# Optimization experiments

Measured on AMD Instinct MI355X. Metric: run time of the kernel, lower is better.

## Reference

```python
import jax, jax.numpy as jnp
import numpy as np
import math

D, S, B = 64, 2048, 16  # head_dim, seq_len, batch (inputs stored as [D, S, B])


def setup_inputs() -> dict:
    key = jax.random.key(0)
    kq, kk, kv = jax.random.split(key, 3)
    return {
        "Q": jax.random.normal(kq, (D, S, B), dtype=jnp.float32),
        "K": jax.random.normal(kk, (D, S, B), dtype=jnp.float32),
        "V": jax.random.normal(kv, (D, S, B), dtype=jnp.float32),
        "d_k": S,
    }


def reference(Q, K, V, d_k):
    # transpose(0, 2): [D, S, B] -> [B, S, D]
    q = jnp.transpose(Q, (2, 1, 0))
    k = jnp.transpose(K, (2, 1, 0))
    v = jnp.transpose(V, (2, 1, 0))
    # bmm(_Q, K_T) * 1/sqrt(d_k): [B, S, S]
    scores = jnp.einsum("bsd,btd->bst", q, k) * (1.0 / math.sqrt(d_k))
    # original does view(-1, d_k) + Softmax over dim=1; with d_k == last dim
    # this is a softmax over the key axis. Dropout is identity in eval mode.
    probs = jax.nn.softmax(scores, axis=-1)
    out = jnp.einsum("bst,btd->bsd", probs, v)  # [B, S, D]
    # transpose(0, 2) back: [D, S, B]
    return jnp.transpose(out, (2, 1, 0))
```

## Files before the change

kernel.cpp:

```cpp
#include <hip/hip_runtime.h>

#define D_ 64
#define S_ 2048
#define B_ 16
#define QT 64
#define KVT 128

typedef short short8 __attribute__((ext_vector_type(8)));
typedef short short4a __attribute__((ext_vector_type(4)));
typedef float floatx4 __attribute__((ext_vector_type(4)));
typedef unsigned uint2v __attribute__((ext_vector_type(2)));
typedef unsigned uint4v __attribute__((ext_vector_type(4)));

#define SC2 (1.4426950408889634f / 45.254833995939045f)

__device__ __forceinline__ unsigned short f2bf(float f) {
  unsigned u = __builtin_bit_cast(unsigned, f);
  u += 0x7fffu + ((u >> 16) & 1u);
  return (unsigned short)(u >> 16);
}

__global__ __launch_bounds__(256) void pack_all(const float* __restrict__ Q,
                                                const float* __restrict__ K,
                                                const float* __restrict__ V,
                                                unsigned short* __restrict__ Qp,
                                                unsigned short* __restrict__ Kp,
                                                unsigned short* __restrict__ Vt) {
  __shared__ __align__(16) unsigned short tile[256][72];
  const int t = threadIdx.x;
  const int bid = blockIdx.x;
  if (bid < 256) {
    const bool isK = bid >= 128;
    const float* src = isK ? K : Q;
    unsigned short* dst = isK ? Kp : Qp;
    const float scale = isK ? SC2 : 1.0f;
    const int rb = bid & 127;
    const int s0 = rb * 16;
#pragma unroll
    for (int i = 0; i < 16; i++) {
      int j = i * 256 + t;
      int d = j >> 6;
      int sb4 = (j & 63) * 4;
      const float4 v = *(const float4*)(src + (size_t)d * (S_ * B_) + s0 * B_ + sb4);
      float vv[4] = {v.x, v.y, v.z, v.w};
#pragma unroll
      for (int k = 0; k < 4; k++) {
        int sb = sb4 + k;
        tile[(sb & 15) * 16 + (sb >> 4)][d] = f2bf(vv[k] * scale);
      }
    }
    __syncthreads();
#pragma unroll
    for (int i = 0; i < 8; i++) {
      int j = i * 256 + t;
      int r = j >> 3, c = j & 7;
      int b = r >> 4, si = r & 15;
      uint4 v = *(const uint4*)(&tile[r][c * 8]);
      *(uint4*)(dst + (((size_t)(b * 128 + rb)) << 10) + ((c >> 2) << 9) +
                (((c & 3) * 16 + si) << 3)) = v;
    }
  } else {
    const int vb = bid - 256;
    const int s0 = (vb & 31) * 64;
    const int d0 = (vb >> 5) * 16;
    const int dblk = vb >> 5;
#pragma unroll
    for (int i = 0; i < 16; i++) {
      int j = i * 256 + t;
      int dd = j >> 8;
      int sb4 = (j & 255) * 4;
      const float4 v = *(const float4*)(V + (size_t)(d0 + dd) * (S_ * B_) + s0 * B_ + sb4);
      float vv[4] = {v.x, v.y, v.z, v.w};
#pragma unroll
      for (int k = 0; k < 4; k++) {
        int sb = sb4 + k;
        tile[(sb & 15) * 16 + dd][sb >> 4] = f2bf(vv[k]);
      }
    }
    __syncthreads();
#pragma unroll
    for (int i = 0; i < 8; i++) {
      int j = i * 256 + t;
      int b = j >> 7;
      int c32r = (j >> 6) & 1;
      int l = j & 63, g = l >> 4, ln = l & 15;
      const unsigned short* row = &tile[b * 16 + ln][c32r * 32];
      uint2 u0 = *(const uint2*)(row + g * 4);
      uint2 u1 = *(const uint2*)(row + 16 + g * 4);
      int c32 = (s0 >> 5) + c32r;
      uint4 o = make_uint4(u0.x, u0.y, u1.x, u1.y);
      *(uint4*)(Vt + (((size_t)(b * 64 + c32) * 4 + dblk) << 9) + l * 8) = o;
    }
  }
}

__global__ __launch_bounds__(256, 2) void attn(const unsigned short* __restrict__ Qp,
                                               const unsigned short* __restrict__ Kp,
                                               const unsigned short* __restrict__ Vt,
                                               float* __restrict__ Ot) {
  __shared__ __align__(16) char smem_[69632 + 1024];
  float* red = (float*)smem_;
  float* lred = (float*)(smem_ + 69632);

  const int tid = threadIdx.x;
  const int w = tid >> 6, l = tid & 63, g = l >> 4, ln = l & 15;
  const int b = blockIdx.x & 15;
  const int q0 = (int)(blockIdx.x >> 4) * QT;

  const unsigned short* Qb = Qp + ((size_t)b << 17);
  const unsigned short* Kb = Kp + ((size_t)b << 17);
  const unsigned short* Vb = Vt + ((size_t)b << 17);

  const unsigned short* Qw = Qb + (((size_t)(q0 >> 4)) << 10) + l * 8;
  const unsigned short* Kw = Kb + w * 2048 + l * 8;
  const unsigned short* Vw = Vb + w * 2048 + l * 8;

  short8 qf[4][2];
#pragma unroll
  for (int nf = 0; nf < 4; nf++)
#pragma unroll
    for (int ks = 0; ks < 2; ks++)
      qf[nf][ks] = *(const short8*)(Qw + nf * 1024 + ks * 512);

  short8 kf[2][2];
#pragma unroll
  for (int mf = 0; mf < 2; mf++)
#pragma unroll
    for (int ks = 0; ks < 2; ks++)
      kf[mf][ks] = *(const short8*)(Kw + mf * 1024 + ks * 512);

  short8 vf[4];
#pragma unroll
  for (int mfd = 0; mfd < 4; mfd++)
    vf[mfd] = *(const short8*)(Vw + mfd * 512);

  const short8 ones8 = {(short)0x3F80, (short)0x3F80, (short)0x3F80, (short)0x3F80,
                        (short)0x3F80, (short)0x3F80, (short)0x3F80, (short)0x3F80};
  floatx4 oacc[4][4];
  floatx4 dacc[4];
#pragma unroll
  for (int mfd = 0; mfd < 4; mfd++)
#pragma unroll
    for (int nf = 0; nf < 4; nf++) oacc[mfd][nf] = (floatx4){0.f, 0.f, 0.f, 0.f};
#pragma unroll
  for (int nf = 0; nf < 4; nf++) dacc[nf] = (floatx4){0.f, 0.f, 0.f, 0.f};

  for (int t = 0; t < 16; t++) {
    const int tn = ((t + 1) & 15) * 8192;

    floatx4 sacc[2][4];
#pragma unroll
    for (int mf = 0; mf < 2; mf++)
#pragma unroll
      for (int nf = 0; nf < 4; nf++) sacc[mf][nf] = (floatx4){0.f, 0.f, 0.f, 0.f};
    __builtin_amdgcn_s_setprio(1);
#pragma unroll
    for (int ks = 0; ks < 2; ks++)
#pragma unroll
      for (int mf = 0; mf < 2; mf++)
#pragma unroll
        for (int nf = 0; nf < 4; nf++)
          sacc[mf][nf] = __builtin_amdgcn_mfma_f32_16x16x32_bf16(kf[mf][ks], qf[nf][ks],
                                                                 sacc[mf][nf], 0, 0, 0);
    __builtin_amdgcn_s_setprio(0);

#pragma unroll
    for (int mf = 0; mf < 2; mf++)
#pragma unroll
      for (int ks = 0; ks < 2; ks++)
        kf[mf][ks] = *(const short8*)(Kw + tn + mf * 1024 + ks * 512);

    short8 pbf[4];
#pragma unroll
    for (int nf = 0; nf < 4; nf++) {
      uint2v pu[2];
#pragma unroll
      for (int mf = 0; mf < 2; mf++) {
        unsigned u0 = __builtin_bit_cast(unsigned, __builtin_amdgcn_exp2f(sacc[mf][nf][0])) + 0x8000u;
        unsigned u1 = __builtin_bit_cast(unsigned, __builtin_amdgcn_exp2f(sacc[mf][nf][1])) + 0x8000u;
        unsigned u2 = __builtin_bit_cast(unsigned, __builtin_amdgcn_exp2f(sacc[mf][nf][2])) + 0x8000u;
        unsigned u3 = __builtin_bit_cast(unsigned, __builtin_amdgcn_exp2f(sacc[mf][nf][3])) + 0x8000u;
        unsigned lo = __builtin_amdgcn_perm(u1, u0, 0x07060302u);
        unsigned hi = __builtin_amdgcn_perm(u3, u2, 0x07060302u);
        pu[mf] = (uint2v){lo, hi};
      }
      pbf[nf] = __builtin_bit_cast(short8, (uint4v){pu[0][0], pu[0][1], pu[1][0], pu[1][1]});
    }

    __builtin_amdgcn_s_setprio(1);
#pragma unroll
    for (int nf = 0; nf < 4; nf++)
      dacc[nf] = __builtin_amdgcn_mfma_f32_16x16x32_bf16(ones8, pbf[nf], dacc[nf], 0, 0, 0);

#pragma unroll
    for (int mfd = 0; mfd < 4; mfd++)
#pragma unroll
      for (int nf = 0; nf < 4; nf++)
        oacc[mfd][nf] = __builtin_amdgcn_mfma_f32_16x16x32_bf16(vf[mfd], pbf[nf],
                                                                oacc[mfd][nf], 0, 0, 0);
    __builtin_amdgcn_s_setprio(0);

#pragma unroll
    for (int mfd = 0; mfd < 4; mfd++)
      vf[mfd] = *(const short8*)(Vw + tn + mfd * 512);
  }

  if (g == 0) {
#pragma unroll
    for (int nf = 0; nf < 4; nf++) lred[w * 64 + nf * 16 + ln] = dacc[nf][0];
  }
#pragma unroll
  for (int mfd = 0; mfd < 4; mfd++)
#pragma unroll
    for (int nf = 0; nf < 4; nf++)
      *(floatx4*)(&red[w * 4352 + (nf * 16 + ln) * 68 + mfd * 16 + g * 4]) = oacc[mfd][nf];
  __syncthreads();

  const int q = l;
  const float denom = lred[q] + lred[64 + q] + lred[128 + q] + lred[192 + q];
  const float linv = 1.0f / denom;
#pragma unroll
  for (int i = 0; i < 4; i++) {
    floatx4 s = (floatx4){0.f, 0.f, 0.f, 0.f};
#pragma unroll
    for (int w2 = 0; w2 < 4; w2++)
      s += *(const floatx4*)(&red[w2 * 4352 + q * 68 + w * 16 + i * 4]);
    s *= linv;
#pragma unroll
    for (int r = 0; r < 4; r++)
      Ot[(size_t)(b * D_ + w * 16 + i * 4 + r) * S_ + q0 + q] = s[r];
  }
}

__global__ __launch_bounds__(256) void unpack_o(const float* __restrict__ Ot,
                                                float* __restrict__ out) {
  const int d0 = (int)(blockIdx.x & 7) * 8;
  const int s0 = (int)(blockIdx.x >> 3) * 64;
  __shared__ float u[8 * 1024];
  const int t = threadIdx.x;
#pragma unroll
  for (int i = 0; i < 8; i++) {
    int j = i * 256 + t;
    int d = j >> 8, bb = (j >> 4) & 15, c = j & 15;
    float4 v = *(const float4*)(Ot + (size_t)(bb * D_ + d0 + d) * S_ + s0 + c * 4);
    float vv[4] = {v.x, v.y, v.z, v.w};
#pragma unroll
    for (int k = 0; k < 4; k++) {
      int si = c * 4 + k;
      int W = si * 16 + bb;
      int Wp = W ^ ((si & 15) << 2);
      u[d * 1024 + Wp] = vv[k];
    }
  }
  __syncthreads();
#pragma unroll
  for (int i = 0; i < 8; i++) {
    int j = i * 256 + t;
    int d = j >> 8, c2 = j & 255;
    int G = c2 ^ ((c2 >> 2) & 15);
    float4 v = *(const float4*)(&u[d * 1024 + G * 4]);
    *(float4*)(out + (size_t)(d0 + d) * (S_ * B_) + s0 * B_ + c2 * 4) = v;
  }
}

extern "C" void kernel_launch(void* const* d_in, const int* in_sizes, int n_in,
                              void* d_out, int out_size, void* d_ws, size_t ws_size,
                              hipStream_t stream) {
  const float* Q = (const float*)d_in[0];
  const float* K = (const float*)d_in[1];
  const float* V = (const float*)d_in[2];
  float* out = (float*)d_out;
  char* ws = (char*)d_ws;
  unsigned short* Qp = (unsigned short*)(ws);
  unsigned short* Kp = (unsigned short*)(ws + (4u << 20));
  unsigned short* Vt = (unsigned short*)(ws + (8u << 20));
  float* Ot = (float*)(ws + (12u << 20));

  hipLaunchKernelGGL(pack_all, dim3(384), dim3(256), 0, stream, Q, K, V, Qp, Kp, Vt);
  hipLaunchKernelGGL(attn, dim3(512), dim3(256), 0, stream, Qp, Kp, Vt, Ot);
  hipLaunchKernelGGL(unpack_o, dim3(256), dim3(256), 0, stream, Ot, out);
}
```

Measured before the change: 100.0 us.

## Double query tile per block to 8 waves and halve LDS reduction buffer

Each attention block now handles 128 queries with 512 threads: two groups of four waves, each group splitting the key range four ways for its own 64-query half. The cross-wave output reduction is restructured into a two-stage add in shared memory, using half-sized buffers per query half, which cuts LDS use per query and removes the four-way reads in the final pass. The intent is to halve the block count and keep per-block LDS bounded so more waves stay resident. The cost is an extra barrier and read-modify-write traffic in the reduction.

```diff
diff --git a/kernel.cpp b/kernel.cpp
--- a/kernel.cpp
+++ b/kernel.cpp
@@ -3,11 +3,10 @@
 #define D_ 64
 #define S_ 2048
 #define B_ 16
-#define QT 64
+#define QT 128
 #define KVT 128
 
 typedef short short8 __attribute__((ext_vector_type(8)));
-typedef short short4a __attribute__((ext_vector_type(4)));
 typedef float floatx4 __attribute__((ext_vector_type(4)));
 typedef unsigned uint2v __attribute__((ext_vector_type(2)));
 typedef unsigned uint4v __attribute__((ext_vector_type(4)));
@@ -94,16 +93,16 @@
   }
 }
 
-__global__ __launch_bounds__(256, 2) void attn(const unsigned short* __restrict__ Qp,
+__global__ __launch_bounds__(512, 2) void attn(const unsigned short* __restrict__ Qp,
                                                const unsigned short* __restrict__ Kp,
                                                const unsigned short* __restrict__ Vt,
                                                float* __restrict__ Ot) {
-  __shared__ __align__(16) char smem_[69632 + 1024];
-  float* red = (float*)smem_;
-  float* lred = (float*)(smem_ + 69632);
+  __shared__ __align__(16) float red[2][2][64][68];
+  __shared__ float lred[2][4][64];
 
   const int tid = threadIdx.x;
   const int w = tid >> 6, l = tid & 63, g = l >> 4, ln = l & 15;
+  const int qh = w >> 2, ksw = w & 3;
   const int b = blockIdx.x & 15;
   const int q0 = (int)(blockIdx.x >> 4) * QT;
 
@@ -111,9 +110,9 @@
   const unsigned short* Kb = Kp + ((size_t)b << 17);
   const unsigned short* Vb = Vt + ((size_t)b << 17);
 
-  const unsigned short* Qw = Qb + (((size_t)(q0 >> 4)) << 10) + l * 8;
-  const unsigned short* Kw = Kb + w * 2048 + l * 8;
-  const unsigned short* Vw = Vb + w * 2048 + l * 8;
+  const unsigned short* Qw = Qb + (((size_t)((q0 >> 4) + qh * 4)) << 10) + l * 8;
+  const unsigned short* Kw = Kb + ksw * 2048 + l * 8;
+  const unsigned short* Vw = Vb + ksw * 2048 + l * 8;
 
   short8 qf[4][2];
 #pragma unroll
@@ -207,28 +206,39 @@
 
   if (g == 0) {
 #pragma unroll
-    for (int nf = 0; nf < 4; nf++) lred[w * 64 + nf * 16 + ln] = dacc[nf][0];
-  }
-#pragma unroll
-  for (int mfd = 0; mfd < 4; mfd++)
-#pragma unroll
-    for (int nf = 0; nf < 4; nf++)
-      *(floatx4*)(&red[w * 4352 + (nf * 16 + ln) * 68 + mfd * 16 + g * 4]) = oacc[mfd][nf];
+    for (int nf = 0; nf < 4; nf++) lred[qh][ksw][nf * 16 + ln] = dacc[nf][0];
+  }
+  if (ksw < 2) {
+#pragma unroll
+    for (int mfd = 0; mfd < 4; mfd++)
+#pragma unroll
+      for (int nf = 0; nf < 4; nf++)
+        *(floatx4*)(&red[qh][ksw][nf * 16 + ln][mfd * 16 + g * 4]) = oacc[mfd][nf];
+  }
   __syncthreads();
+  if (ksw >= 2) {
+#pragma unroll
+    for (int mfd = 0; mfd < 4; mfd++)
+#pragma unroll
+      for (int nf = 0; nf < 4; nf++) {
+        float* p = &red[qh][ksw - 2][nf * 16 + ln][mfd * 16 + g * 4];
+        *(floatx4*)p = *(const floatx4*)p + oacc[mfd][nf];
+      }
+  }
+  __syncthreads();
 
   const int q = l;
-  const float denom = lred[q] + lred[64 + q] + lred[128 + q] + lred[192 + q];
+  const float denom = lred[qh][0][q] + lred[qh][1][q] + lred[qh][2][q] + lred[qh][3][q];
   const float linv = 1.0f / denom;
+  const int dq = ksw;
 #pragma unroll
   for (int i = 0; i < 4; i++) {
-    floatx4 s = (floatx4){0.f, 0.f, 0.f, 0.f};
-#pragma unroll
-    for (int w2 = 0; w2 < 4; w2++)
-      s += *(const floatx4*)(&red[w2 * 4352 + q * 68 + w * 16 + i * 4]);
+    floatx4 s = *(const floatx4*)(&red[qh][0][q][dq * 16 + i * 4]) +
+                *(const floatx4*)(&red[qh][1][q][dq * 16 + i * 4]);
     s *= linv;
 #pragma unroll
     for (int r = 0; r < 4; r++)
-      Ot[(size_t)(b * D_ + w * 16 + i * 4 + r) * S_ + q0 + q] = s[r];
+      Ot[(size_t)(b * D_ + dq * 16 + i * 4 + r) * S_ + q0 + qh * 64 + q] = s[r];
   }
 }
 
@@ -277,6 +287,6 @@
   float* Ot = (float*)(ws + (12u << 20));
 
   hipLaunchKernelGGL(pack_all, dim3(384), dim3(256), 0, stream, Q, K, V, Qp, Kp, Vt);
-  hipLaunchKernelGGL(attn, dim3(512), dim3(256), 0, stream, Qp, Kp, Vt, Ot);
+  hipLaunchKernelGGL(attn, dim3(256), dim3(512), 0, stream, Qp, Kp, Vt, Ot);
   hipLaunchKernelGGL(unpack_o, dim3(256), dim3(256), 0, stream, Ot, out);
 }
```

Measured after the change: 101.7 us. About the same (+1.7%).
